# Kernel tuning notes

Hardware: AMD Instinct MI355X
Metric: run time of the kernel (lower is better)

The kernel has to match this reference:

```python
import jax, jax.numpy as jnp
import numpy as np

N = 6144
IN_F = 128
OUT_F = 128
H = 4
OUT_PER_HEAD = OUT_F // H  # 32
ALPHA = 0.2  # leaky relu slope
NEG_BIG = -9e15


def setup_inputs() -> dict:
    key = jax.random.key(0)
    k1, k2, k3, k4 = jax.random.split(key, 4)
    h_mat = jax.random.normal(k1, (N, IN_F), dtype=jnp.float32)
    adj = (jax.random.uniform(k2, (N, N)) < 0.05).astype(jnp.float32)
    # glorot-ish scaled params
    weight = jax.random.normal(k3, (IN_F, H * OUT_PER_HEAD), dtype=jnp.float32) * (1.0 / np.sqrt(IN_F))
    att_weight = jax.random.normal(k4, (H, 2 * OUT_PER_HEAD), dtype=jnp.float32) * (1.0 / np.sqrt(OUT_PER_HEAD))
    return {"h_mat": h_mat, "adj": adj, "weight": weight, "att_weight": att_weight}


def reference(h_mat, adj, weight, att_weight):
    n = h_mat.shape[0]
    # W h : [n, H, f]
    wh = jnp.matmul(h_mat, weight).reshape(n, H, OUT_PER_HEAD)
    a_src = att_weight[:, :OUT_PER_HEAD]   # [H, f]
    a_dst = att_weight[:, OUT_PER_HEAD:]   # [H, f]
    logit_parent = jnp.einsum("nhf,hf->nh", wh, a_src)  # [n, H]
    logit_child = jnp.einsum("nhf,hf->nh", wh, a_dst)   # [n, H]
    # e_{ij,h} = leaky_relu(parent_i + child_j) : [n, n, H]
    e = jax.nn.leaky_relu(logit_parent[:, None, :] + logit_child[None, :, :], ALPHA)
    att = jnp.where(adj[..., None] > 0, e, NEG_BIG)
    att = jax.nn.softmax(att, axis=1)  # softmax over source nodes j
    # dropout is identity in inference mode (enable_dropout=False)
    h_prime = jnp.einsum("njh,jhf->nhf", att, wh)
    return h_prime.reshape(n, -1)  # concat=True -> [n, out_features]
```

## Files before the change

kernel.cpp:

```cpp
#include <hip/hip_runtime.h>
#include <hip/hip_bf16.h>
#include <stdint.h>
#include <stddef.h>

#define GN 6144
#define GH 4
#define HALF 3072
#define MAXD2 256

typedef float    f32x2  __attribute__((ext_vector_type(2)));
typedef float    f32x4  __attribute__((ext_vector_type(4)));
typedef float    f32x16 __attribute__((ext_vector_type(16)));
typedef unsigned u32x4  __attribute__((ext_vector_type(4)));
typedef __bf16   bf16x4 __attribute__((ext_vector_type(4)));
typedef __bf16   bf16x8 __attribute__((ext_vector_type(8)));

__device__ __forceinline__ float fast_exp2(float x) {
#if __has_builtin(__builtin_amdgcn_exp2f)
  return __builtin_amdgcn_exp2f(x);
#else
  return exp2f(x);
#endif
}

__global__ __launch_bounds__(256) void gat_wh(const float* __restrict__ hm,
                                              const float* __restrict__ wgt,
                                              const float* __restrict__ aw,
                                              __bf16* __restrict__ whR,
                                              float* __restrict__ lp2,
                                              float* __restrict__ lc2) {
  __shared__ float ldsC[64 * 132];
  const int t = threadIdx.x;
  const int wave = t >> 6, lane = t & 63;
  const int col = lane & 31, kg = lane >> 5;
  const int n0 = blockIdx.x * 64;
  const int rowHalf = (wave & 1) * 32;
  const int colBase = (wave >> 1) * 64;

  f32x16 acc[2];
#pragma unroll
  for (int ct = 0; ct < 2; ++ct)
#pragma unroll
    for (int i = 0; i < 16; ++i) acc[ct][i] = 0.0f;

#pragma unroll
  for (int kk = 0; kk < 8; ++kk) {
    const int k = kk * 16 + kg * 8;
    const f32x4 h0 = *(const f32x4*)(hm + (size_t)(n0 + rowHalf + col) * 128 + k);
    const f32x4 h1 = *(const f32x4*)(hm + (size_t)(n0 + rowHalf + col) * 128 + k + 4);
    bf16x8 af;
#pragma unroll
    for (int e = 0; e < 4; ++e) { af[e] = (__bf16)h0[e]; af[e + 4] = (__bf16)h1[e]; }
#pragma unroll
    for (int ct = 0; ct < 2; ++ct) {
      bf16x8 bfr;
#pragma unroll
      for (int e = 0; e < 8; ++e)
        bfr[e] = (__bf16)wgt[(size_t)(k + e) * 128 + colBase + ct * 32 + col];
      acc[ct] = __builtin_amdgcn_mfma_f32_32x32x16_bf16(af, bfr, acc[ct], 0, 0, 0);
    }
  }
#pragma unroll
  for (int ct = 0; ct < 2; ++ct)
#pragma unroll
    for (int r = 0; r < 16; ++r)
      ldsC[(rowHalf + (r & 3) + 8 * (r >> 2) + 4 * kg) * 132 + colBase + ct * 32 + col] =
          acc[ct][r];
  __syncthreads();

  {
    const int rr = t >> 2, cg = (t & 3) * 32;
    __bf16* dst = whR + (size_t)(n0 + rr) * 128 + cg;
#pragma unroll
    for (int q = 0; q < 4; ++q) {
      bf16x8 v;
#pragma unroll
      for (int e = 0; e < 8; ++e) v[e] = (__bf16)ldsC[rr * 132 + cg + q * 8 + e];
      *(bf16x8*)(dst + q * 8) = v;
    }
  }
  {
    const int nl = t & 63, h = t >> 6;
    float sp = 0.f, sd = 0.f;
#pragma unroll
    for (int f = 0; f < 32; ++f) {
      const float v = ldsC[nl * 132 + h * 32 + f];
      sp = fmaf(v, aw[h * 64 + f], sp);
      sd = fmaf(v, aw[h * 64 + 32 + f], sd);
    }
    const float LOG2E = 1.4426950408889634f;
    lp2[(n0 + nl) * GH + h] = sp * LOG2E;
    lc2[(n0 + nl) * GH + h] = sd * LOG2E;
  }
}

__global__ __launch_bounds__(256) void gat_fused(const float* __restrict__ adj,
                                                 const __bf16* __restrict__ whR,
                                                 const float* __restrict__ lp2,
                                                 const float* __restrict__ lc2,
                                                 float* __restrict__ out) {
  __shared__ unsigned short jidx[4][MAXD2];
  __shared__ __bf16 elsb[4][MAXD2 * GH];
  __shared__ float accx[4][16][8];
  __shared__ float denx[4][4];
  const int t = threadIdx.x, wave = t >> 6, lane = t & 63;
  const int row = blockIdx.x * 2 + (wave >> 1);
  const int half = wave & 1;
  const float* arow = adj + (size_t)row * GN + half * HALF;

  unsigned base = 0;
  f32x4 buf[4];
#pragma unroll
  for (int c = 0; c < 4; ++c) buf[c] = *(const f32x4*)(arow + c * 256 + lane * 4);
#pragma unroll 4
  for (int c = 0; c < 12; ++c) {
    const f32x4 a = buf[c & 3];
    if (c + 4 < 12) buf[c & 3] = *(const f32x4*)(arow + (c + 4) * 256 + lane * 4);
#pragma unroll
    for (int s = 0; s < 4; ++s) {
      const bool p = a[s] > 0.f;
      const unsigned long long m = __ballot(p);
      const unsigned rank = (unsigned)__popcll(m & ((1ull << lane) - 1ull));
      const unsigned pos = base + rank;
      if (p && pos < MAXD2)
        jidx[wave][pos] = (unsigned short)(half * HALF + c * 256 + lane * 4 + s);
      base += (unsigned)__popcll(m);
    }
  }
  int dg = (int)base;
  if (dg > MAXD2) dg = MAXD2;
  for (int k = dg + lane; k < MAXD2; k += 64) jidx[wave][k] = 0;

  const f32x4 lpv = *(const f32x4*)(lp2 + (size_t)row * GH);
  f32x2 d01 = f32x2{0.f, 0.f}, d23 = f32x2{0.f, 0.f};
  const int nch = (dg + 63) >> 6;
  for (int c = 0; c < nch; ++c) {
    const int k = c * 64 + lane;
    const bool valid = k < dg;
    const int jv = valid ? (int)jidx[wave][k] : 0;
    const f32x4 lc = *(const f32x4*)(lc2 + (size_t)jv * GH);

    f32x2 x01 = f32x2{lpv[0] + lc[0], lpv[1] + lc[1]};
    f32x2 x23 = f32x2{lpv[2] + lc[2], lpv[3] + lc[3]};
    x01 = __builtin_elementwise_max(x01, x01 * 0.2f);
    x23 = __builtin_elementwise_max(x23, x23 * 0.2f);
    const float vf = valid ? 1.f : 0.f;
    const f32x2 e01 = f32x2{fast_exp2(x01[0]), fast_exp2(x01[1])} * vf;
    const f32x2 e23 = f32x2{fast_exp2(x23[0]), fast_exp2(x23[1])} * vf;
    d01 += e01; d23 += e23;
    bf16x4 ep;
    ep[0] = (__bf16)e01[0]; ep[1] = (__bf16)e01[1];
    ep[2] = (__bf16)e23[0]; ep[3] = (__bf16)e23[1];
    *(bf16x4*)&elsb[wave][k * 4] = ep;
  }

  const int qlane = lane & 15;
  const int elane = lane >> 4;
  const int hsel = qlane >> 2;
  f32x4 accA = f32x4{0.f, 0.f, 0.f, 0.f};
  f32x4 accB = f32x4{0.f, 0.f, 0.f, 0.f};

  const int ngrp = (dg + 3) >> 2;
#pragma unroll 4
  for (int g = 0; g < ngrp; ++g) {
    const int es = g * 4 + elane;
    const int jj = (int)jidx[wave][es];
    const u32x4 wb = *(const u32x4*)(whR + (size_t)jj * 128 + qlane * 8);
    const float eb = (float)elsb[wave][es * 4 + hsel];
#pragma unroll
    for (int w = 0; w < 4; ++w) {
      const float wlo = __uint_as_float(wb[w] << 16);
      const float whi = __uint_as_float(wb[w] & 0xffff0000u);
      if (w < 2) {
        accA[2 * w]     = fmaf(eb, wlo, accA[2 * w]);
        accA[2 * w + 1] = fmaf(eb, whi, accA[2 * w + 1]);
      } else {
        accB[2 * w - 4] = fmaf(eb, wlo, accB[2 * w - 4]);
        accB[2 * w - 3] = fmaf(eb, whi, accB[2 * w - 3]);
      }
    }
  }

#pragma unroll
  for (int off = 16; off <= 32; off <<= 1) {
#pragma unroll
    for (int e = 0; e < 4; ++e) {
      accA[e] += __shfl_xor(accA[e], off);
      accB[e] += __shfl_xor(accB[e], off);
    }
  }
  f32x4 dv = f32x4{d01[0], d01[1], d23[0], d23[1]};
#pragma unroll
  for (int off = 1; off < 64; off <<= 1) {
    dv[0] += __shfl_xor(dv[0], off);
    dv[1] += __shfl_xor(dv[1], off);
    dv[2] += __shfl_xor(dv[2], off);
    dv[3] += __shfl_xor(dv[3], off);
  }

  if (lane < 16) {
    *(f32x4*)&accx[wave][qlane][0] = accA;
    *(f32x4*)&accx[wave][qlane][4] = accB;
  }
  if (lane == 0) *(f32x4*)&denx[wave][0] = dv;
  __syncthreads();
  if ((wave & 1) == 0 && lane < 16) {
    const f32x4 pA = *(const f32x4*)&accx[wave + 1][qlane][0];
    const f32x4 pB = *(const f32x4*)&accx[wave + 1][qlane][4];
    const float den = denx[wave][hsel] + denx[wave + 1][hsel];
    const float inv = 1.0f / den;
    *(f32x4*)(out + (size_t)row * 128 + qlane * 8)     = (accA + pA) * inv;
    *(f32x4*)(out + (size_t)row * 128 + qlane * 8 + 4) = (accB + pB) * inv;
  }
}

extern "C" void kernel_launch(void* const* d_in, const int* in_sizes, int n_in,
                              void* d_out, int out_size, void* d_ws, size_t ws_size,
                              hipStream_t stream) {
  const float* hm  = (const float*)d_in[0];
  const float* adj = (const float*)d_in[1];
  const float* wgt = (const float*)d_in[2];
  const float* aw  = (const float*)d_in[3];
  float* out = (float*)d_out;

  char* ws = (char*)d_ws;
  __bf16* whR = (__bf16*)ws; ws += (size_t)GN * 128 * 2;
  float* lp2  = (float*)ws;  ws += GN * GH * 4;
  float* lc2  = (float*)ws;  ws += GN * GH * 4;

  gat_wh<<<96, 256, 0, stream>>>(hm, wgt, aw, whR, lp2, lc2);
  gat_fused<<<GN / 2, 256, 0, stream>>>(adj, whR, lp2, lc2, out);
}
```

Baseline: 55.50 us.

## Process two rows per block and overlap second row's adjacency scan with first row's gather

Each block now handles four rows, two per wave pair, in sequence. The ballot-compaction scan of the second row's adjacency is interleaved into the first row's weighted-gather loop, one chunk every few iterations, so global adjacency loads overlap gather work. This is meant to hide the latency of streaming the dense adjacency matrix. In exchange the block count is halved, register pressure rises, and per-block work becomes more serial.

```diff
diff --git a/kernel.cpp b/kernel.cpp
--- a/kernel.cpp
+++ b/kernel.cpp
@@ -99,47 +99,53 @@
                                                  const float* __restrict__ lp2,
                                                  const float* __restrict__ lc2,
                                                  float* __restrict__ out) {
-  __shared__ unsigned short jidx[4][MAXD2];
+  __shared__ unsigned short jidx[4][2][MAXD2];
   __shared__ __bf16 elsb[4][MAXD2 * GH];
   __shared__ float accx[4][16][8];
   __shared__ float denx[4][4];
   const int t = threadIdx.x, wave = t >> 6, lane = t & 63;
-  const int row = blockIdx.x * 2 + (wave >> 1);
+  const int r0 = blockIdx.x * 4 + (wave >> 1);
+  const int r1 = r0 + 2;
   const int half = wave & 1;
-  const float* arow = adj + (size_t)row * GN + half * HALF;
-
-  unsigned base = 0;
-  f32x4 buf[4];
-#pragma unroll
-  for (int c = 0; c < 4; ++c) buf[c] = *(const f32x4*)(arow + c * 256 + lane * 4);
+  const float* arow0 = adj + (size_t)r0 * GN + half * HALF;
+  const float* arow1 = adj + (size_t)r1 * GN + half * HALF;
+  const int qlane = lane & 15;
+  const int elane = lane >> 4;
+  const int hsel = qlane >> 2;
+
+  unsigned base0 = 0;
+  {
+    f32x4 buf[4];
+#pragma unroll
+    for (int c = 0; c < 4; ++c) buf[c] = *(const f32x4*)(arow0 + c * 256 + lane * 4);
 #pragma unroll 4
-  for (int c = 0; c < 12; ++c) {
-    const f32x4 a = buf[c & 3];
-    if (c + 4 < 12) buf[c & 3] = *(const f32x4*)(arow + (c + 4) * 256 + lane * 4);
-#pragma unroll
-    for (int s = 0; s < 4; ++s) {
-      const bool p = a[s] > 0.f;
-      const unsigned long long m = __ballot(p);
-      const unsigned rank = (unsigned)__popcll(m & ((1ull << lane) - 1ull));
-      const unsigned pos = base + rank;
-      if (p && pos < MAXD2)
-        jidx[wave][pos] = (unsigned short)(half * HALF + c * 256 + lane * 4 + s);
-      base += (unsigned)__popcll(m);
-    }
-  }
-  int dg = (int)base;
-  if (dg > MAXD2) dg = MAXD2;
-  for (int k = dg + lane; k < MAXD2; k += 64) jidx[wave][k] = 0;
-
-  const f32x4 lpv = *(const f32x4*)(lp2 + (size_t)row * GH);
+    for (int c = 0; c < 12; ++c) {
+      const f32x4 a = buf[c & 3];
+      if (c + 4 < 12) buf[c & 3] = *(const f32x4*)(arow0 + (c + 4) * 256 + lane * 4);
+#pragma unroll
+      for (int s = 0; s < 4; ++s) {
+        const bool p = a[s] > 0.f;
+        const unsigned long long m = __ballot(p);
+        const unsigned rank = (unsigned)__popcll(m & ((1ull << lane) - 1ull));
+        const unsigned pos = base0 + rank;
+        if (p && pos < MAXD2)
+          jidx[wave][0][pos] = (unsigned short)(half * HALF + c * 256 + lane * 4 + s);
+        base0 += (unsigned)__popcll(m);
+      }
+    }
+  }
+  int dg0 = (int)base0;  if (dg0 > MAXD2) dg0 = MAXD2;
+  for (int k = dg0 + lane; k < MAXD2; k += 64) jidx[wave][0][k] = 0;
+
+  const f32x4 lpv = *(const f32x4*)(lp2 + (size_t)r0 * GH);
+
   f32x2 d01 = f32x2{0.f, 0.f}, d23 = f32x2{0.f, 0.f};
-  const int nch = (dg + 63) >> 6;
-  for (int c = 0; c < nch; ++c) {
+#pragma unroll
+  for (int c = 0; c < 4; ++c) {
     const int k = c * 64 + lane;
-    const bool valid = k < dg;
-    const int jv = valid ? (int)jidx[wave][k] : 0;
+    const bool valid = k < dg0;
+    const int jv = valid ? (int)jidx[wave][0][k] : 0;
     const f32x4 lc = *(const f32x4*)(lc2 + (size_t)jv * GH);
-
     f32x2 x01 = f32x2{lpv[0] + lc[0], lpv[1] + lc[1]};
     f32x2 x23 = f32x2{lpv[2] + lc[2], lpv[3] + lc[3]};
     x01 = __builtin_elementwise_max(x01, x01 * 0.2f);
@@ -154,41 +160,68 @@
     *(bf16x4*)&elsb[wave][k * 4] = ep;
   }
 
-  const int qlane = lane & 15;
-  const int elane = lane >> 4;
-  const int hsel = qlane >> 2;
+  unsigned base1 = 0;
+  int c1 = 0, cd = 0;
+  f32x4 bA = *(const f32x4*)(arow1 + 0 * 256 + lane * 4);
+  f32x4 bB = *(const f32x4*)(arow1 + 1 * 256 + lane * 4);
+  f32x4 bC = *(const f32x4*)(arow1 + 2 * 256 + lane * 4);
+  f32x4 bD = *(const f32x4*)(arow1 + 3 * 256 + lane * 4);
+
+#define T1_CHUNK()                                                             \
+  do {                                                                         \
+    const f32x4 a = bA;                                                        \
+    _Pragma("unroll")                                                          \
+    for (int s = 0; s < 4; ++s) {                                              \
+      const bool p = a[s] > 0.f;                                               \
+      const unsigned long long m = __ballot(p);                                \
+      const unsigned rank = (unsigned)__popcll(m & ((1ull << lane) - 1ull));   \
+      const unsigned pos = base1 + rank;                                       \
+      if (p && pos < MAXD2)                                                    \
+        jidx[wave][1][pos] =                                                   \
+            (unsigned short)(half * HALF + c1 * 256 + lane * 4 + s);           \
+      base1 += (unsigned)__popcll(m);                                          \
+    }                                                                          \
+    bA = bB; bB = bC; bC = bD;                                                 \
+    if (c1 + 4 < 12) bD = *(const f32x4*)(arow1 + (c1 + 4) * 256 + lane * 4);  \
+    ++c1;                                                                      \
+  } while (0)
+
   f32x4 accA = f32x4{0.f, 0.f, 0.f, 0.f};
   f32x4 accB = f32x4{0.f, 0.f, 0.f, 0.f};
-
-  const int ngrp = (dg + 3) >> 2;
-#pragma unroll 4
-  for (int g = 0; g < ngrp; ++g) {
-    const int es = g * 4 + elane;
-    const int jj = (int)jidx[wave][es];
-    const u32x4 wb = *(const u32x4*)(whR + (size_t)jj * 128 + qlane * 8);
-    const float eb = (float)elsb[wave][es * 4 + hsel];
-#pragma unroll
-    for (int w = 0; w < 4; ++w) {
-      const float wlo = __uint_as_float(wb[w] << 16);
-      const float whi = __uint_as_float(wb[w] & 0xffff0000u);
-      if (w < 2) {
-        accA[2 * w]     = fmaf(eb, wlo, accA[2 * w]);
-        accA[2 * w + 1] = fmaf(eb, whi, accA[2 * w + 1]);
-      } else {
-        accB[2 * w - 4] = fmaf(eb, wlo, accB[2 * w - 4]);
-        accB[2 * w - 3] = fmaf(eb, whi, accB[2 * w - 3]);
+  {
+    const int ngrp = (dg0 + 3) >> 2;
+    for (int g = 0; g < ngrp; ++g) {
+      if (cd == 0 && c1 < 12) { T1_CHUNK(); cd = 3; }
+      --cd;
+      const int es = g * 4 + elane;
+      const int jj = (int)jidx[wave][0][es];
+      const u32x4 wb = *(const u32x4*)(whR + (size_t)jj * 128 + qlane * 8);
+      const float eb = (float)elsb[wave][es * 4 + hsel];
+#pragma unroll
+      for (int w = 0; w < 4; ++w) {
+        const float wlo = __uint_as_float(wb[w] << 16);
+        const float whi = __uint_as_float(wb[w] & 0xffff0000u);
+        if (w < 2) {
+          accA[2 * w]     = fmaf(eb, wlo, accA[2 * w]);
+          accA[2 * w + 1] = fmaf(eb, whi, accA[2 * w + 1]);
+        } else {
+          accB[2 * w - 4] = fmaf(eb, wlo, accB[2 * w - 4]);
+          accB[2 * w - 3] = fmaf(eb, whi, accB[2 * w - 3]);
+        }
       }
     }
-  }
-
-#pragma unroll
-  for (int off = 16; off <= 32; off <<= 1) {
+    while (c1 < 12) T1_CHUNK();
+  }
+  int dg1 = (int)base1;  if (dg1 > MAXD2) dg1 = MAXD2;
+  for (int k = dg1 + lane; k < MAXD2; k += 64) jidx[wave][1][k] = 0;
+
+#pragma unroll
+  for (int off = 16; off <= 32; off <<= 1)
 #pragma unroll
     for (int e = 0; e < 4; ++e) {
       accA[e] += __shfl_xor(accA[e], off);
       accB[e] += __shfl_xor(accB[e], off);
     }
-  }
   f32x4 dv = f32x4{d01[0], d01[1], d23[0], d23[1]};
 #pragma unroll
   for (int off = 1; off < 64; off <<= 1) {
@@ -197,7 +230,6 @@
     dv[2] += __shfl_xor(dv[2], off);
     dv[3] += __shfl_xor(dv[3], off);
   }
-
   if (lane < 16) {
     *(f32x4*)&accx[wave][qlane][0] = accA;
     *(f32x4*)&accx[wave][qlane][4] = accB;
@@ -209,9 +241,86 @@
     const f32x4 pB = *(const f32x4*)&accx[wave + 1][qlane][4];
     const float den = denx[wave][hsel] + denx[wave + 1][hsel];
     const float inv = 1.0f / den;
-    *(f32x4*)(out + (size_t)row * 128 + qlane * 8)     = (accA + pA) * inv;
-    *(f32x4*)(out + (size_t)row * 128 + qlane * 8 + 4) = (accB + pB) * inv;
-  }
+    *(f32x4*)(out + (size_t)r0 * 128 + qlane * 8)     = (accA + pA) * inv;
+    *(f32x4*)(out + (size_t)r0 * 128 + qlane * 8 + 4) = (accB + pB) * inv;
+  }
+  __syncthreads();
+
+  const f32x4 lpv1 = *(const f32x4*)(lp2 + (size_t)r1 * GH);
+  d01 = f32x2{0.f, 0.f}; d23 = f32x2{0.f, 0.f};
+#pragma unroll
+  for (int c = 0; c < 4; ++c) {
+    const int k = c * 64 + lane;
+    const bool valid = k < dg1;
+    const int jv = valid ? (int)jidx[wave][1][k] : 0;
+    const f32x4 lc = *(const f32x4*)(lc2 + (size_t)jv * GH);
+    f32x2 x01 = f32x2{lpv1[0] + lc[0], lpv1[1] + lc[1]};
+    f32x2 x23 = f32x2{lpv1[2] + lc[2], lpv1[3] + lc[3]};
+    x01 = __builtin_elementwise_max(x01, x01 * 0.2f);
+    x23 = __builtin_elementwise_max(x23, x23 * 0.2f);
+    const float vf = valid ? 1.f : 0.f;
+    const f32x2 e01 = f32x2{fast_exp2(x01[0]), fast_exp2(x01[1])} * vf;
+    const f32x2 e23 = f32x2{fast_exp2(x23[0]), fast_exp2(x23[1])} * vf;
+    d01 += e01; d23 += e23;
+    bf16x4 ep;
+    ep[0] = (__bf16)e01[0]; ep[1] = (__bf16)e01[1];
+    ep[2] = (__bf16)e23[0]; ep[3] = (__bf16)e23[1];
+    *(bf16x4*)&elsb[wave][k * 4] = ep;
+  }
+  accA = f32x4{0.f, 0.f, 0.f, 0.f};
+  accB = f32x4{0.f, 0.f, 0.f, 0.f};
+  {
+    const int ngrp = (dg1 + 3) >> 2;
+#pragma unroll 4
+    for (int g = 0; g < ngrp; ++g) {
+      const int es = g * 4 + elane;
+      const int jj = (int)jidx[wave][1][es];
+      const u32x4 wb = *(const u32x4*)(whR + (size_t)jj * 128 + qlane * 8);
+      const float eb = (float)elsb[wave][es * 4 + hsel];
+#pragma unroll
+      for (int w = 0; w < 4; ++w) {
+        const float wlo = __uint_as_float(wb[w] << 16);
+        const float whi = __uint_as_float(wb[w] & 0xffff0000u);
+        if (w < 2) {
+          accA[2 * w]     = fmaf(eb, wlo, accA[2 * w]);
+          accA[2 * w + 1] = fmaf(eb, whi, accA[2 * w + 1]);
+        } else {
+          accB[2 * w - 4] = fmaf(eb, wlo, accB[2 * w - 4]);
+          accB[2 * w - 3] = fmaf(eb, whi, accB[2 * w - 3]);
+        }
+      }
+    }
+  }
+#pragma unroll
+  for (int off = 16; off <= 32; off <<= 1)
+#pragma unroll
+    for (int e = 0; e < 4; ++e) {
+      accA[e] += __shfl_xor(accA[e], off);
+      accB[e] += __shfl_xor(accB[e], off);
+    }
+  dv = f32x4{d01[0], d01[1], d23[0], d23[1]};
+#pragma unroll
+  for (int off = 1; off < 64; off <<= 1) {
+    dv[0] += __shfl_xor(dv[0], off);
+    dv[1] += __shfl_xor(dv[1], off);
+    dv[2] += __shfl_xor(dv[2], off);
+    dv[3] += __shfl_xor(dv[3], off);
+  }
+  if (lane < 16) {
+    *(f32x4*)&accx[wave][qlane][0] = accA;
+    *(f32x4*)&accx[wave][qlane][4] = accB;
+  }
+  if (lane == 0) *(f32x4*)&denx[wave][0] = dv;
+  __syncthreads();
+  if ((wave & 1) == 0 && lane < 16) {
+    const f32x4 pA = *(const f32x4*)&accx[wave + 1][qlane][0];
+    const f32x4 pB = *(const f32x4*)&accx[wave + 1][qlane][4];
+    const float den = denx[wave][hsel] + denx[wave + 1][hsel];
+    const float inv = 1.0f / den;
+    *(f32x4*)(out + (size_t)r1 * 128 + qlane * 8)     = (accA + pA) * inv;
+    *(f32x4*)(out + (size_t)r1 * 128 + qlane * 8 + 4) = (accB + pB) * inv;
+  }
+#undef T1_CHUNK
 }
 
 extern "C" void kernel_launch(void* const* d_in, const int* in_sizes, int n_in,
@@ -229,5 +338,5 @@
   float* lc2  = (float*)ws;  ws += GN * GH * 4;
 
   gat_wh<<<96, 256, 0, stream>>>(hm, wgt, aw, whR, lp2, lc2);
-  gat_fused<<<GN / 2, 256, 0, stream>>>(adj, whR, lp2, lc2, out);
+  gat_fused<<<GN / 4, 256, 0, stream>>>(adj, whR, lp2, lc2, out);
 }
```

After: 76.69 us. 1.38x slower.
